# Kernel tuning notes

Hardware: AMD Instinct MI355X
Metric: run time of the kernel (lower is better)

Reference implementation:

```python
import jax, jax.numpy as jnp
import numpy as np

VAR0, VAR1 = 0.1, 0.2
THRESHOLD = 0.35
NEGPOS_RATIO = 7
LOW_GT_THRESH = 0.2  # match() filters GT whose best prior IoU < 0.2


def setup_inputs() -> dict:
    key = jax.random.key(0)
    ks = jax.random.split(key, 8)
    B, P, G = 16, 43008, 128
    loc_data = jax.random.normal(ks[0], (B, P, 4), jnp.float32)
    conf_data = jax.random.normal(ks[1], (B, P, 2), jnp.float32)
    landm_data = jax.random.normal(ks[2], (B, P, 10), jnp.float32)
    # priors in cxcywh form, positive sizes
    pc = jax.random.uniform(ks[3], (P, 2), jnp.float32)
    pwh = jax.random.uniform(ks[4], (P, 2), jnp.float32, minval=0.02, maxval=0.32)
    priors = jnp.concatenate([pc, pwh], axis=1)
    # targets: valid xyxy boxes + 10 landmark coords + label (face=1)
    ctr = jax.random.uniform(ks[5], (B, G, 2), jnp.float32, minval=0.2, maxval=0.8)
    wh = jax.random.uniform(ks[6], (B, G, 2), jnp.float32, minval=0.05, maxval=0.3)
    boxes = jnp.concatenate([ctr - wh / 2, ctr + wh / 2], axis=-1)
    landms = jax.random.uniform(ks[7], (B, G, 10), jnp.float32)
    labels = jnp.ones((B, G, 1), jnp.float32)
    targets = jnp.concatenate([boxes, landms, labels], axis=-1)
    return {"loc_data": loc_data, "conf_data": conf_data, "landm_data": landm_data,
            "priors": priors, "targets": targets}


def point_form(priors):
    return jnp.concatenate([priors[:, :2] - priors[:, 2:] / 2,
                            priors[:, :2] + priors[:, 2:] / 2], axis=1)


def jaccard(a, b):  # a: [G,4] xyxy, b: [P,4] xyxy -> [G,P]
    lt = jnp.maximum(a[:, None, :2], b[None, :, :2])
    rb = jnp.minimum(a[:, None, 2:], b[None, :, 2:])
    wh = jnp.clip(rb - lt, 0.0)
    inter = wh[..., 0] * wh[..., 1]
    area_a = (a[:, 2] - a[:, 0]) * (a[:, 3] - a[:, 1])
    area_b = (b[:, 2] - b[:, 0]) * (b[:, 3] - b[:, 1])
    return inter / (area_a[:, None] + area_b[None, :] - inter)


def encode(matched, priors):  # matched xyxy [P,4], priors cxcywh [P,4]
    g_cxcy = (matched[:, :2] + matched[:, 2:]) / 2 - priors[:, :2]
    g_cxcy = g_cxcy / (VAR0 * priors[:, 2:])
    g_wh = jnp.log((matched[:, 2:] - matched[:, :2]) / priors[:, 2:]) / VAR1
    return jnp.concatenate([g_cxcy, g_wh], axis=1)


def encode_landm(matched, priors):  # matched [P,10], priors [P,4]
    m = matched.reshape(-1, 5, 2)
    g = (m - priors[:, None, :2]) / (VAR0 * priors[:, None, 2:])
    return g.reshape(-1, 10)


def match_one(truths, labels, landms, priors):
    G = truths.shape[0]
    overlaps = jaccard(truths, point_form(priors))  # [G, P]
    best_prior_overlap = overlaps.max(axis=1)       # [G]
    best_prior_idx = overlaps.argmax(axis=1)        # [G]
    valid = best_prior_overlap >= LOW_GT_THRESH
    any_valid = jnp.any(valid)
    best_truth_overlap = overlaps.max(axis=0)       # [P]
    best_truth_idx = overlaps.argmax(axis=0)        # [P]
    # index_fill_(0, best_prior_idx_filter, 2): ensure each valid GT keeps its best prior
    fill_val = jnp.where(valid, 2.0, best_truth_overlap[best_prior_idx])
    best_truth_overlap = best_truth_overlap.at[best_prior_idx].set(fill_val)
    # best_truth_idx[best_prior_idx[j]] = j for all j
    best_truth_idx = best_truth_idx.at[best_prior_idx].set(jnp.arange(G))
    matches = truths[best_truth_idx]                       # [P,4]
    conf = labels[best_truth_idx].astype(jnp.int32)        # [P]
    conf = jnp.where(best_truth_overlap < THRESHOLD, 0, conf)
    conf = jnp.where(any_valid, conf, 0)  # no valid GT -> all background
    loc = encode(matches, priors)
    landm = encode_landm(landms[best_truth_idx], priors)
    return loc, conf, landm


def smooth_l1(x):
    ax = jnp.abs(x)
    return jnp.where(ax < 1.0, 0.5 * ax * ax, ax - 0.5)


def reference(loc_data, conf_data, landm_data, priors, targets):
    truths = targets[..., :4]
    landms = targets[..., 4:14]
    labels = targets[..., 14]
    loc_t, conf_t, landm_t = jax.vmap(
        lambda t, l, lm: match_one(t, l, lm, priors))(truths, labels, landms)

    # landmark loss over positives
    pos1 = conf_t > 0
    N1 = jnp.maximum(pos1.sum().astype(jnp.float32), 1.0)
    loss_landm = jnp.sum(smooth_l1(landm_data - landm_t) * pos1[..., None])

    # localization loss over positives
    pos = conf_t != 0
    num_pos = pos.sum(axis=1, keepdims=True)  # [B,1]
    loss_l = jnp.sum(smooth_l1(loc_data - loc_t) * pos[..., None])

    # hard negative mining on per-prior CE loss
    lse = jax.scipy.special.logsumexp(conf_data, axis=-1)  # [B,P]
    gathered = jnp.take_along_axis(conf_data, conf_t[..., None], axis=-1)[..., 0]
    ce_all = lse - gathered                                # [B,P] per-prior CE
    mine = jnp.where(pos, 0.0, ce_all)
    loss_idx = jnp.argsort(-mine, axis=1)
    idx_rank = jnp.argsort(loss_idx, axis=1)
    num_neg = jnp.clip(NEGPOS_RATIO * num_pos, None, pos.shape[1] - 1)
    neg = idx_rank < num_neg
    sel = pos | neg
    loss_c = jnp.sum(jnp.where(sel, ce_all, 0.0))

    N = jnp.maximum(num_pos.sum().astype(jnp.float32), 1.0)
    return loss_l / N, loss_c / N, loss_landm / N1
```

## Files before the change

kernel.cpp:

```cpp
#include <hip/hip_runtime.h>
#include <stdint.h>


#define GC 8
#define PPI 4

__device__ __forceinline__ float sl1(float x) {
  float a = fabsf(x);
  return a < 1.f ? 0.5f * a * a : a - 0.5f;
}

__device__ __forceinline__ double dwave(double v) {
#pragma unroll
  for (int o = 32; o; o >>= 1) v += __shfl_down(v, o);
  return v;
}

__global__ __launch_bounds__(256) void k_match(
    const float* __restrict__ priors, const float* __restrict__ targets,
    float* __restrict__ bto, int* __restrict__ bti,
    unsigned long long* __restrict__ bp, int P, int G, int NIOU, int PTI,
    int NGC, int PC) {
  int tid = threadIdx.x;
  __shared__ float4 sgt[128];
  __shared__ float sga[128];
  __shared__ unsigned long long sred[GC * 256];

  if ((int)blockIdx.x < NIOU) {
    int b = blockIdx.x / PTI, tile = blockIdx.x % PTI;
    int base = tile * (256 * PPI);
    for (int g = tid; g < G; g += 256) {
      const float* t = targets + ((size_t)b * G + g) * 15;
      float x1 = t[0], y1 = t[1], x2 = t[2], y2 = t[3];
      sgt[g] = make_float4(x1, y1, x2, y2);
      sga[g] = (x2 - x1) * (y2 - y1);
    }
    __syncthreads();

    float px1[PPI], py1[PPI], px2[PPI], py2[PPI], pa[PPI];
    float bi[PPI], sb[PPI];
    int bidx[PPI];
#pragma unroll
    for (int k = 0; k < PPI; ++k) {
      int p = base + tid + k * 256;
      int pl = p < P ? p : P - 1;
      float4 pr = ((const float4*)priors)[pl];
      px1[k] = pr.x - pr.z * 0.5f; py1[k] = pr.y - pr.w * 0.5f;
      px2[k] = pr.x + pr.z * 0.5f; py2[k] = pr.y + pr.w * 0.5f;
      pa[k] = pr.z * pr.w;
      bi[k] = 0.f; sb[k] = 1.f; bidx[k] = 0;
    }

#define IOU_BODY(T, A, GG)                                                 \
  {                                                                        \
    float iw = fminf(T.z, px2[k]) - fmaxf(T.x, px1[k]);                    \
    float ih = fminf(T.w, py2[k]) - fmaxf(T.y, py1[k]);                    \
    float inter = fmaxf(iw, 0.f) * ih;        \
    float S = A + pa[k];                                                   \
    if (inter * sb[k] > bi[k] * S) { bi[k] = inter; sb[k] = S; bidx[k] = GG; } \
  }

    for (int g = 0; g < G; g += 4) {
      float4 T0 = sgt[g], T1 = sgt[g + 1], T2 = sgt[g + 2], T3 = sgt[g + 3];
      float A0 = sga[g], A1 = sga[g + 1], A2 = sga[g + 2], A3 = sga[g + 3];
#pragma unroll
      for (int k = 0; k < PPI; ++k) {
        IOU_BODY(T0, A0, g)
        IOU_BODY(T1, A1, g + 1)
        IOU_BODY(T2, A2, g + 2)
        IOU_BODY(T3, A3, g + 3)
      }
    }
#undef IOU_BODY
#pragma unroll
    for (int k = 0; k < PPI; ++k) {
      int p = base + tid + k * 256;
      if (p < P) {
        bto[(size_t)b * P + p] = bi[k] / (sb[k] - bi[k]);
        bti[(size_t)b * P + p] = bidx[k];
      }
    }
  } else {
    int bc = blockIdx.x - NIOU;
    int pc = bc % PC;
    int gcb = (bc / PC) % NGC;
    int b = bc / (PC * NGC);
    int g0 = gcb * GC;

    if (tid < GC) {
      int g = g0 + tid;
      float4 v = make_float4(0.f, 0.f, 0.f, 0.f);
      if (g < G) {
        const float* t = targets + ((size_t)b * G + g) * 15;
        v = make_float4(t[0], t[1], t[2], t[3]);
      }
      sgt[tid] = v;
    }
    __syncthreads();

    float gx1[GC], gy1[GC], gx2[GC], gy2[GC], ga[GC];
#pragma unroll
    for (int j = 0; j < GC; ++j) {
      float4 T = sgt[j];
      gx1[j] = T.x; gy1[j] = T.y; gx2[j] = T.z; gy2[j] = T.w;
      ga[j] = (T.z - T.x) * (T.w - T.y);
    }

    int chunk = (P + PC - 1) / PC;
    int ps = pc * chunk;
    int pe = ps + chunk; if (pe > P) pe = P;
    int count = pe - ps;

    float bi[GC], sb[GC];
    unsigned bpp[GC];
#pragma unroll
    for (int j = 0; j < GC; ++j) { bi[j] = 0.f; sb[j] = 1.f; bpp[j] = (unsigned)(ps + tid); }

#define BP_BODY(X1, Y1, X2, Y2, AR, PP)                                     \
  {                                                                         \
    float iw = fminf(gx2[j], X2) - fmaxf(gx1[j], X1);                       \
    float ih = fminf(gy2[j], Y2) - fmaxf(gy1[j], Y1);                       \
    float inter = fmaxf(iw, 0.f) * ih;                                      \
    float S = ga[j] + AR;                                                   \
    if (inter * sb[j] > bi[j] * S) { bi[j] = inter; sb[j] = S; bpp[j] = (unsigned)PP; } \
  }

    for (int i = tid; i < count; i += 1024) {
      int p0 = ps + i;
      int i1 = i + 256, i2 = i + 512, i3 = i + 768;
      int p1 = (i1 < count) ? ps + i1 : p0;
      int p2 = (i2 < count) ? ps + i2 : p0;
      int p3 = (i3 < count) ? ps + i3 : p0;
      float4 q0 = ((const float4*)priors)[p0];
      float4 q1 = ((const float4*)priors)[p1];
      float4 q2 = ((const float4*)priors)[p2];
      float4 q3 = ((const float4*)priors)[p3];
      float ax1 = q0.x - q0.z * 0.5f, ay1 = q0.y - q0.w * 0.5f;
      float ax2 = q0.x + q0.z * 0.5f, ay2 = q0.y + q0.w * 0.5f;
      float aa = q0.z * q0.w;
      float bx1 = q1.x - q1.z * 0.5f, by1 = q1.y - q1.w * 0.5f;
      float bx2 = q1.x + q1.z * 0.5f, by2 = q1.y + q1.w * 0.5f;
      float ba = q1.z * q1.w;
      float cx1 = q2.x - q2.z * 0.5f, cy1 = q2.y - q2.w * 0.5f;
      float cx2 = q2.x + q2.z * 0.5f, cy2 = q2.y + q2.w * 0.5f;
      float ca = q2.z * q2.w;
      float dx1 = q3.x - q3.z * 0.5f, dy1 = q3.y - q3.w * 0.5f;
      float dx2 = q3.x + q3.z * 0.5f, dy2 = q3.y + q3.w * 0.5f;
      float da = q3.z * q3.w;
#pragma unroll
      for (int j = 0; j < GC; ++j) {
        BP_BODY(ax1, ay1, ax2, ay2, aa, p0)
        BP_BODY(bx1, by1, bx2, by2, ba, p1)
        BP_BODY(cx1, cy1, cx2, cy2, ca, p2)
        BP_BODY(dx1, dy1, dx2, dy2, da, p3)
      }
    }
#undef BP_BODY

#pragma unroll
    for (int j = 0; j < GC; ++j) {
      float iou = bi[j] / (sb[j] - bi[j]);
      unsigned long long pk =
          ((unsigned long long)__float_as_uint(iou) << 32) | (unsigned)(~bpp[j]);
      sred[j * 256 + tid] = pk;
    }
    __syncthreads();
    {
      int j = tid >> 5, s = tid & 31;
      unsigned long long m = sred[j * 256 + s];
#pragma unroll
      for (int t = 1; t < 8; ++t) {
        unsigned long long v = sred[j * 256 + s + t * 32];
        if (v > m) m = v;
      }
      __syncthreads();
      sred[j * 256 + s] = m;
    }
    __syncthreads();
    if (tid < GC) {
      unsigned long long m = sred[tid * 256];
      for (int s = 1; s < 32; ++s) {
        unsigned long long v = sred[tid * 256 + s];
        if (v > m) m = v;
      }
      int g = g0 + tid;
      if (g < G) atomicMax(&bp[(size_t)b * G + g], m);
    }
  }
}

__global__ void k_scatter(const unsigned long long* __restrict__ bp,
                          float* __restrict__ bto, int* __restrict__ bti,
                          int* __restrict__ anyv, int P, int G) {
  int b = blockIdx.x, g = threadIdx.x;
  __shared__ unsigned spp[128];
  __shared__ int s_any;
  if (g == 0) s_any = 0;
  __syncthreads();
  unsigned long long m = bp[(size_t)b * G + g];
  unsigned pp = ~(unsigned)m;
  float val = __uint_as_float((unsigned)(m >> 32));
  bool ok = (m != 0ULL);
  float oldv = 0.f;
  if (ok) oldv = bto[(size_t)b * P + pp];
  spp[g] = ok ? pp : 0xFFFFFFFFu;
  if (ok && val >= 0.2f) s_any = 1;
  __syncthreads();
  bool win = ok;
  for (int g2 = g + 1; g2 < G; ++g2)
    if (spp[g2] == pp) win = false;
  if (win) {
    bto[(size_t)b * P + pp] = (val >= 0.2f) ? 2.0f : oldv;
    bti[(size_t)b * P + pp] = g;
  }
  __syncthreads();
  if (g == 0) anyv[b] = s_any;
}

__global__ __launch_bounds__(256) void k_main(
    const float* __restrict__ loc, const float* __restrict__ conf,
    const float* __restrict__ lm, const float* __restrict__ priors,
    const float* __restrict__ targets, const float* __restrict__ bto,
    const int* __restrict__ bti, const int* __restrict__ anyv,
    float* __restrict__ mine, unsigned* __restrict__ h1,
    double* __restrict__ pll, double* __restrict__ pllm,
    double* __restrict__ plc, double* __restrict__ msum,
    int* __restrict__ pnp, int P, int G, int PT) {
  int b = blockIdx.x / PT, tile = blockIdx.x % PT;
  int tid = threadIdx.x;
  int p = tile * 256 + tid;

  __shared__ float st[128 * 15];
  __shared__ unsigned hist[1024];
  __shared__ double rs[16];
  __shared__ int ri[4];

  for (int i = tid; i < G * 15; i += 256) st[i] = targets[(size_t)b * G * 15 + i];
  for (int i = tid; i < 1024; i += 256) hist[i] = 0;
  __syncthreads();

  double ll = 0, llm = 0, lc = 0, ms = 0;
  int np = 0;
  if (p < P) {
    size_t idx = (size_t)b * P + p;
    int av = anyv[b];
    float ov = bto[idx];
    int ti = bti[idx];
    bool pos = av && (ov >= 0.35f);

    float2 c = ((const float2*)conf)[idx];
    float mx = fmaxf(c.x, c.y);
    float lse = mx + logf(expf(c.x - mx) + expf(c.y - mx));
    float ce = lse - (pos ? c.y : c.x);
    float mv = pos ? 0.f : ce;
    mine[idx] = mv;
    ms = (double)mv;
    atomicAdd(&hist[__float_as_uint(mv) >> 21], 1u);

    if (pos) {
      np = 1;
      lc = (double)ce;
      float4 pr = ((const float4*)priors)[p];
      const float* t = st + ti * 15;
      float dx = 0.1f * pr.z, dy = 0.1f * pr.w;
      float gx = ((t[0] + t[2]) * 0.5f - pr.x) / dx;
      float gy = ((t[1] + t[3]) * 0.5f - pr.y) / dy;
      float gw = logf((t[2] - t[0]) / pr.z) * 5.0f;
      float gh = logf((t[3] - t[1]) / pr.w) * 5.0f;
      float4 ld = ((const float4*)loc)[idx];
      ll = (double)(sl1(ld.x - gx) + sl1(ld.y - gy) + sl1(ld.z - gw) +
                    sl1(ld.w - gh));
      const float2* lmd = (const float2*)lm + idx * 5;
      float s = 0.f;
#pragma unroll
      for (int j = 0; j < 5; ++j) {
        float2 lv = lmd[j];
        float ex = (t[4 + 2 * j] - pr.x) / dx;
        float ey = (t[5 + 2 * j] - pr.y) / dy;
        s += sl1(lv.x - ex) + sl1(lv.y - ey);
      }
      llm = (double)s;
    }
  }

  ll = dwave(ll);
  llm = dwave(llm);
  lc = dwave(lc);
  ms = dwave(ms);
#pragma unroll
  for (int o = 32; o; o >>= 1) np += __shfl_down(np, o);
  int lane = tid & 63, wid = tid >> 6;
  if (lane == 0) {
    rs[wid] = ll; rs[4 + wid] = llm; rs[8 + wid] = lc; rs[12 + wid] = ms;
    ri[wid] = np;
  }
  __syncthreads();
  if (tid == 0) {
    pll[blockIdx.x] = rs[0] + rs[1] + rs[2] + rs[3];
    pllm[blockIdx.x] = rs[4] + rs[5] + rs[6] + rs[7];
    plc[blockIdx.x] = rs[8] + rs[9] + rs[10] + rs[11];
    msum[blockIdx.x] = rs[12] + rs[13] + rs[14] + rs[15];
    pnp[blockIdx.x] = ri[0] + ri[1] + ri[2] + ri[3];
  }
  for (int i = tid; i < 1024; i += 256)
    if (hist[i]) atomicAdd(&h1[(size_t)b * 1024 + i], hist[i]);
}

__global__ __launch_bounds__(1024) void k_tail(
    const unsigned* __restrict__ h1, const int* __restrict__ pnp,
    const double* __restrict__ msum, const float* __restrict__ mine,
    int* __restrict__ num_pos, double* __restrict__ pfs_b, int P, int PT) {
  int b = blockIdx.x, tid = threadIdx.x;
  __shared__ double sm[1024];
  __shared__ int sn[1024];
  __shared__ unsigned S[1024];
  __shared__ unsigned hs[2048];
  __shared__ int spf1, sk1, spf21, sk2;
  __shared__ unsigned stb;
  __shared__ double stie;
  __shared__ double rs[16];

  int n = 0;
  double m = 0;
  for (int i = tid; i < PT; i += 1024) { n += pnp[b * PT + i]; m += msum[b * PT + i]; }
  sn[tid] = n; sm[tid] = m;
  __syncthreads();
  for (int off = 512; off; off >>= 1) {
    if (tid < off) { sn[tid] += sn[tid + off]; sm[tid] += sm[tid + off]; }
    __syncthreads();
  }
  int npos = sn[0];
  if (tid == 0) num_pos[b] = npos;

  long long k = 7LL * (long long)npos;
  long long cap = P - 1;
  if (k <= 0) return;
  if (k >= cap) {
    if (tid == 0) pfs_b[b] = sm[0];
    return;
  }

  const float* mrow = mine + (size_t)b * P;

  {
    unsigned own = h1[(size_t)b * 1024 + tid];
    S[tid] = own;
    __syncthreads();
    for (int off = 1; off < 1024; off <<= 1) {
      unsigned add = (tid + off < 1024) ? S[tid + off] : 0;
      __syncthreads();
      S[tid] += add;
      __syncthreads();
    }
    int cnt = __syncthreads_count((long long)S[tid] >= k);
    int seg = cnt - 1;
    if (tid == seg) {
      long long cum = (seg + 1 < 1024) ? (long long)S[seg + 1] : 0;
      spf1 = seg;
      sk1 = (int)(k - cum);
    }
  }
  __syncthreads();
  int pf = spf1;

  hs[tid] = 0; hs[tid + 1024] = 0;
  __syncthreads();
  for (int base = 0; base < P; base += 4096) {
    int i0 = base + tid;
    int i1 = i0 + 1024, i2 = i0 + 2048, i3 = i0 + 3072;
    unsigned b0 = (i0 < P) ? __float_as_uint(mrow[i0]) : 0u;
    unsigned b1 = (i1 < P) ? __float_as_uint(mrow[i1]) : 0u;
    unsigned b2 = (i2 < P) ? __float_as_uint(mrow[i2]) : 0u;
    unsigned b3 = (i3 < P) ? __float_as_uint(mrow[i3]) : 0u;
    if (i0 < P && (int)(b0 >> 21) == pf) atomicAdd(&hs[(b0 >> 10) & 2047], 1u);
    if (i1 < P && (int)(b1 >> 21) == pf) atomicAdd(&hs[(b1 >> 10) & 2047], 1u);
    if (i2 < P && (int)(b2 >> 21) == pf) atomicAdd(&hs[(b2 >> 10) & 2047], 1u);
    if (i3 < P && (int)(b3 >> 21) == pf) atomicAdd(&hs[(b3 >> 10) & 2047], 1u);
  }
  __syncthreads();
  {
    unsigned h0 = hs[tid * 2], h1v = hs[tid * 2 + 1];
    S[tid] = h0 + h1v;
    __syncthreads();
    for (int off = 1; off < 1024; off <<= 1) {
      unsigned add = (tid + off < 1024) ? S[tid + off] : 0;
      __syncthreads();
      S[tid] += add;
      __syncthreads();
    }
    long long kk = (long long)sk1;
    int cnt = __syncthreads_count((long long)S[tid] >= kk);
    int seg = cnt - 1;
    if (tid == seg) {
      long long cum = (seg + 1 < 1024) ? (long long)S[seg + 1] : 0;
      int bin = seg * 2;
      if (cum + h1v >= kk) bin = seg * 2 + 1;
      else cum += h1v;
      spf21 = (pf << 11) | bin;
      sk2 = (int)(kk - cum);
    }
  }
  __syncthreads();
  int pf21 = spf21;

  hs[tid] = 0;
  __syncthreads();
  for (int base = 0; base < P; base += 4096) {
    int i0 = base + tid;
    int i1 = i0 + 1024, i2 = i0 + 2048, i3 = i0 + 3072;
    unsigned b0 = (i0 < P) ? __float_as_uint(mrow[i0]) : 0u;
    unsigned b1 = (i1 < P) ? __float_as_uint(mrow[i1]) : 0u;
    unsigned b2 = (i2 < P) ? __float_as_uint(mrow[i2]) : 0u;
    unsigned b3 = (i3 < P) ? __float_as_uint(mrow[i3]) : 0u;
    if (i0 < P && (int)(b0 >> 10) == pf21) atomicAdd(&hs[b0 & 1023], 1u);
    if (i1 < P && (int)(b1 >> 10) == pf21) atomicAdd(&hs[b1 & 1023], 1u);
    if (i2 < P && (int)(b2 >> 10) == pf21) atomicAdd(&hs[b2 & 1023], 1u);
    if (i3 < P && (int)(b3 >> 10) == pf21) atomicAdd(&hs[b3 & 1023], 1u);
  }
  __syncthreads();
  {
    unsigned own = hs[tid];
    S[tid] = own;
    __syncthreads();
    for (int off = 1; off < 1024; off <<= 1) {
      unsigned add = (tid + off < 1024) ? S[tid + off] : 0;
      __syncthreads();
      S[tid] += add;
      __syncthreads();
    }
    long long kk = (long long)sk2;
    int cnt = __syncthreads_count((long long)S[tid] >= kk);
    int seg = cnt - 1;
    if (tid == seg) {
      long long cum = (seg + 1 < 1024) ? (long long)S[seg + 1] : 0;
      unsigned tb = ((unsigned)pf21 << 10) | (unsigned)seg;
      stb = tb;
      stie = (double)(kk - cum) * (double)__uint_as_float(tb);
    }
  }
  __syncthreads();

  unsigned tb = stb;
  double v = 0.0;
  for (int base = 0; base < P; base += 4096) {
    int i0 = base + tid;
    int i1 = i0 + 1024, i2 = i0 + 2048, i3 = i0 + 3072;
    unsigned b0 = (i0 < P) ? __float_as_uint(mrow[i0]) : 0u;
    unsigned b1 = (i1 < P) ? __float_as_uint(mrow[i1]) : 0u;
    unsigned b2 = (i2 < P) ? __float_as_uint(mrow[i2]) : 0u;
    unsigned b3 = (i3 < P) ? __float_as_uint(mrow[i3]) : 0u;
    if (b0 > tb) v += (double)__uint_as_float(b0);
    if (b1 > tb) v += (double)__uint_as_float(b1);
    if (b2 > tb) v += (double)__uint_as_float(b2);
    if (b3 > tb) v += (double)__uint_as_float(b3);
  }
  v = dwave(v);
  int lane = tid & 63, wid = tid >> 6;
  if (lane == 0) rs[wid] = v;
  __syncthreads();
  if (tid == 0) {
    double t = 0;
    for (int i = 0; i < 16; ++i) t += rs[i];
    pfs_b[b] = t + stie;
  }
}

__global__ __launch_bounds__(256) void k_fin(
    const double* __restrict__ pll, const double* __restrict__ pllm,
    const double* __restrict__ plc, const double* __restrict__ pfs_b,
    const int* __restrict__ num_pos, float* __restrict__ out, int NBm, int B) {
  int tid = threadIdx.x;
  double a = 0, c = 0, d = 0, f = 0, n = 0;
  for (int i = tid; i < NBm; i += 256) { a += pll[i]; c += pllm[i]; d += plc[i]; }
  for (int i = tid; i < B; i += 256) { f += pfs_b[i]; n += (double)num_pos[i]; }
  a = dwave(a); c = dwave(c); d = dwave(d); f = dwave(f); n = dwave(n);
  __shared__ double rs[5 * 4];
  int lane = tid & 63, wid = tid >> 6;
  if (lane == 0) {
    rs[wid] = a; rs[4 + wid] = c; rs[8 + wid] = d;
    rs[12 + wid] = f; rs[16 + wid] = n;
  }
  __syncthreads();
  if (tid == 0) {
    double A = rs[0] + rs[1] + rs[2] + rs[3];
    double C = rs[4] + rs[5] + rs[6] + rs[7];
    double D = rs[8] + rs[9] + rs[10] + rs[11];
    double F = rs[12] + rs[13] + rs[14] + rs[15];
    double N = rs[16] + rs[17] + rs[18] + rs[19];
    if (N < 1.0) N = 1.0;
    out[0] = (float)(A / N);
    out[1] = (float)((D + F) / N);
    out[2] = (float)(C / N);
  }
}

extern "C" void kernel_launch(void* const* d_in, const int* in_sizes, int n_in,
                              void* d_out, int out_size, void* d_ws,
                              size_t ws_size, hipStream_t stream) {
  const float* loc = (const float*)d_in[0];
  const float* conf = (const float*)d_in[1];
  const float* lm = (const float*)d_in[2];
  const float* priors = (const float*)d_in[3];
  const float* targets = (const float*)d_in[4];

  int P = in_sizes[3] / 4;
  int B = in_sizes[0] / (4 * P);
  int G = in_sizes[4] / (15 * B);
  int PT = (P + 255) / 256;
  int PTI = (P + 256 * PPI - 1) / (256 * PPI);
  int NBm = B * PT;
  int NGC = (G + GC - 1) / GC;
  int PC = 8;
  int NIOU = B * PTI;
  int NBP = B * NGC * PC;

  char* w = (char*)d_ws;
  size_t off = 0;
  unsigned long long* bp = (unsigned long long*)(w + off);
  off += (size_t)B * G * 8;
  double* pfs_b = (double*)(w + off);
  off += (size_t)B * 8;
  int* ctrl = (int*)(w + off);
  off += (size_t)(2 * B) * 4;
  int* anyv = ctrl;
  int* num_pos = ctrl + B;
  unsigned* h1 = (unsigned*)(w + off);
  off += (size_t)B * 1024 * 4;
  size_t clear_bytes = off;
  off = (off + 255) & ~(size_t)255;
  float* bto = (float*)(w + off);
  off += (size_t)B * P * 4;
  int* bti = (int*)(w + off);
  off += (size_t)B * P * 4;
  float* mine = (float*)(w + off);
  off += (size_t)B * P * 4;
  double* pll = (double*)(w + off);
  off += (size_t)NBm * 8;
  double* pllm = (double*)(w + off);
  off += (size_t)NBm * 8;
  double* plc = (double*)(w + off);
  off += (size_t)NBm * 8;
  double* msum = (double*)(w + off);
  off += (size_t)NBm * 8;
  int* pnp = (int*)(w + off);
  off += (size_t)NBm * 4;

  hipMemsetAsync(d_ws, 0, clear_bytes, stream);

  k_match<<<NIOU + NBP, 256, 0, stream>>>(priors, targets, bto, bti, bp, P, G,
                                          NIOU, PTI, NGC, PC);
  k_scatter<<<B, G, 0, stream>>>(bp, bto, bti, anyv, P, G);
  k_main<<<B * PT, 256, 0, stream>>>(loc, conf, lm, priors, targets, bto, bti,
                                     anyv, mine, h1, pll, pllm, plc, msum, pnp,
                                     P, G, PT);
  k_tail<<<B, 1024, 0, stream>>>(h1, pnp, msum, mine, num_pos, pfs_b, P, PT);
  k_fin<<<1, 256, 0, stream>>>(pll, pllm, plc, pfs_b, num_pos, (float*)d_out,
                               NBm, B);
}
```

Measured before the change: 178.8 us.

## Fuse per-prior loss computation into IoU match kernel with delta correction pass

The per-prior loss work (CE, mining value, loc and landmark smooth-L1) now runs in the IoU matching blocks right after best-GT selection, which removes the separate k_main pass that re-read bto/bti. A new k_fix kernel applies the forced best-prior matches afterwards by computing per-batch deltas (old versus new assignment) to the partial sums and patching the mining array. The mining histogram moves into k_tail, which rescans the mine row itself, and final reduction work shifts into k_tail, leaving k_fin with only per-batch values. This trades one full launch and memory pass for a histogram rescan and delta bookkeeping, and the fused IoU blocks now run more memory work alongside the compute-bound matching.

Result: no change. 177.9 us (-0.5%).

```diff
diff --git a/kernel.cpp b/kernel.cpp
--- a/kernel.cpp
+++ b/kernel.cpp
@@ -16,19 +16,28 @@
   return v;
 }
 
-__global__ __launch_bounds__(256) void k_match(
+__global__ __launch_bounds__(256) void k_mm(
     const float* __restrict__ priors, const float* __restrict__ targets,
-    float* __restrict__ bto, int* __restrict__ bti,
-    unsigned long long* __restrict__ bp, int P, int G, int NIOU, int PTI,
-    int NGC, int PC) {
+    const float* __restrict__ loc, const float* __restrict__ conf,
+    const float* __restrict__ lm, float* __restrict__ bto,
+    int* __restrict__ bti, unsigned long long* __restrict__ bp,
+    float* __restrict__ mine, double* __restrict__ pll,
+    double* __restrict__ pllm, double* __restrict__ plc,
+    double* __restrict__ msum, int* __restrict__ pnp, int P, int G, int NIOU,
+    int PTI, int NGC, int PC) {
   int tid = threadIdx.x;
+  __shared__ char smem[16384];
   __shared__ float4 sgt[128];
   __shared__ float sga[128];
-  __shared__ unsigned long long sred[GC * 256];
 
   if ((int)blockIdx.x < NIOU) {
+    float* st = (float*)smem;
+    double* rs = (double*)(smem + 7680);
+    int* ri = (int*)(smem + 7808);
     int b = blockIdx.x / PTI, tile = blockIdx.x % PTI;
     int base = tile * (256 * PPI);
+    for (int i = tid; i < G * 15; i += 256)
+      st[i] = targets[(size_t)b * G * 15 + i];
     for (int g = tid; g < G; g += 256) {
       const float* t = targets + ((size_t)b * G + g) * 15;
       float x1 = t[0], y1 = t[1], x2 = t[2], y2 = t[3];
@@ -55,11 +64,10 @@
   {                                                                        \
     float iw = fminf(T.z, px2[k]) - fmaxf(T.x, px1[k]);                    \
     float ih = fminf(T.w, py2[k]) - fmaxf(T.y, py1[k]);                    \
-    float inter = fmaxf(iw, 0.f) * ih;        \
+    float inter = fmaxf(iw, 0.f) * ih;                                     \
     float S = A + pa[k];                                                   \
     if (inter * sb[k] > bi[k] * S) { bi[k] = inter; sb[k] = S; bidx[k] = GG; } \
   }
-
     for (int g = 0; g < G; g += 4) {
       float4 T0 = sgt[g], T1 = sgt[g + 1], T2 = sgt[g + 2], T3 = sgt[g + 3];
       float A0 = sga[g], A1 = sga[g + 1], A2 = sga[g + 2], A3 = sga[g + 3];
@@ -72,15 +80,73 @@
       }
     }
 #undef IOU_BODY
+
+    double ll = 0, llm = 0, lc = 0, ms = 0;
+    int np = 0;
 #pragma unroll
     for (int k = 0; k < PPI; ++k) {
       int p = base + tid + k * 256;
       if (p < P) {
-        bto[(size_t)b * P + p] = bi[k] / (sb[k] - bi[k]);
-        bti[(size_t)b * P + p] = bidx[k];
+        size_t idx = (size_t)b * P + p;
+        float ov = bi[k] / (sb[k] - bi[k]);
+        int ti = bidx[k];
+        bto[idx] = ov;
+        bti[idx] = ti;
+        bool pos = ov >= 0.35f;
+        float2 c = ((const float2*)conf)[idx];
+        float mx = fmaxf(c.x, c.y);
+        float dd = fabsf(c.x - c.y);
+        float lse = mx + logf(1.f + expf(-dd));
+        float ce = lse - (pos ? c.y : c.x);
+        float mv = pos ? 0.f : ce;
+        mine[idx] = mv;
+        ms += (double)mv;
+        if (pos) {
+          np++;
+          lc += (double)ce;
+          float4 pr = ((const float4*)priors)[p];
+          const float* t = st + ti * 15;
+          float rz = 1.f / pr.z, rw = 1.f / pr.w;
+          float rdx = 10.f * rz, rdy = 10.f * rw;
+          float gx = ((t[0] + t[2]) * 0.5f - pr.x) * rdx;
+          float gy = ((t[1] + t[3]) * 0.5f - pr.y) * rdy;
+          float gw = logf((t[2] - t[0]) * rz) * 5.0f;
+          float gh = logf((t[3] - t[1]) * rw) * 5.0f;
+          float4 ld = ((const float4*)loc)[idx];
+          ll += (double)(sl1(ld.x - gx) + sl1(ld.y - gy) + sl1(ld.z - gw) +
+                         sl1(ld.w - gh));
+          const float2* lmd = (const float2*)lm + idx * 5;
+          float s = 0.f;
+#pragma unroll
+          for (int j = 0; j < 5; ++j) {
+            float2 lv = lmd[j];
+            float ex = (t[4 + 2 * j] - pr.x) * rdx;
+            float ey = (t[5 + 2 * j] - pr.y) * rdy;
+            s += sl1(lv.x - ex) + sl1(lv.y - ey);
+          }
+          llm += (double)s;
+        }
       }
     }
+
+    ll = dwave(ll); llm = dwave(llm); lc = dwave(lc); ms = dwave(ms);
+#pragma unroll
+    for (int o = 32; o; o >>= 1) np += __shfl_down(np, o);
+    int lane = tid & 63, wid = tid >> 6;
+    if (lane == 0) {
+      rs[wid] = ll; rs[4 + wid] = llm; rs[8 + wid] = lc; rs[12 + wid] = ms;
+      ri[wid] = np;
+    }
+    __syncthreads();
+    if (tid == 0) {
+      pll[blockIdx.x] = rs[0] + rs[1] + rs[2] + rs[3];
+      pllm[blockIdx.x] = rs[4] + rs[5] + rs[6] + rs[7];
+      plc[blockIdx.x] = rs[8] + rs[9] + rs[10] + rs[11];
+      msum[blockIdx.x] = rs[12] + rs[13] + rs[14] + rs[15];
+      pnp[blockIdx.x] = ri[0] + ri[1] + ri[2] + ri[3];
+    }
   } else {
+    unsigned long long* sred = (unsigned long long*)smem;
     int bc = blockIdx.x - NIOU;
     int pc = bc % PC;
     int gcb = (bc / PC) % NGC;
@@ -124,7 +190,6 @@
     float S = ga[j] + AR;                                                   \
     if (inter * sb[j] > bi[j] * S) { bi[j] = inter; sb[j] = S; bpp[j] = (unsigned)PP; } \
   }
-
     for (int i = tid; i < count; i += 1024) {
       int p0 = ps + i;
       int i1 = i + 256, i2 = i + 512, i3 = i + 768;
@@ -189,162 +254,184 @@
   }
 }
 
-__global__ void k_scatter(const unsigned long long* __restrict__ bp,
-                          float* __restrict__ bto, int* __restrict__ bti,
-                          int* __restrict__ anyv, int P, int G) {
+__global__ void k_fix(const unsigned long long* __restrict__ bp,
+                      const float* __restrict__ bto, const int* __restrict__ bti,
+                      const float* __restrict__ conf, const float* __restrict__ loc,
+                      const float* __restrict__ lm, const float* __restrict__ priors,
+                      const float* __restrict__ targets, float* __restrict__ mine,
+                      int* __restrict__ anyv, double* __restrict__ dacc,
+                      int* __restrict__ dnpb, int P, int G) {
   int b = blockIdx.x, g = threadIdx.x;
   __shared__ unsigned spp[128];
-  __shared__ int s_any;
-  if (g == 0) s_any = 0;
-  __syncthreads();
+  __shared__ double sd[128 * 4];
+  __shared__ int si[128];
+
   unsigned long long m = bp[(size_t)b * G + g];
   unsigned pp = ~(unsigned)m;
   float val = __uint_as_float((unsigned)(m >> 32));
-  bool ok = (m != 0ULL);
-  float oldv = 0.f;
-  if (ok) oldv = bto[(size_t)b * P + pp];
-  spp[g] = ok ? pp : 0xFFFFFFFFu;
-  if (ok && val >= 0.2f) s_any = 1;
-  __syncthreads();
-  bool win = ok;
+  spp[g] = pp;
+  bool valid = val >= 0.2f;
+  int av = __syncthreads_or(valid ? 1 : 0);
+  if (g == 0) anyv[b] = av;
+
+  bool win = true;
   for (int g2 = g + 1; g2 < G; ++g2)
-    if (spp[g2] == pp) win = false;
+    if (spp[g2] == pp) { win = false; break; }
+
+  double dll = 0, dllm = 0, dlc = 0, dms = 0;
+  int dnp = 0;
   if (win) {
-    bto[(size_t)b * P + pp] = (val >= 0.2f) ? 2.0f : oldv;
-    bti[(size_t)b * P + pp] = g;
-  }
-  __syncthreads();
-  if (g == 0) anyv[b] = s_any;
-}
-
-__global__ __launch_bounds__(256) void k_main(
-    const float* __restrict__ loc, const float* __restrict__ conf,
-    const float* __restrict__ lm, const float* __restrict__ priors,
-    const float* __restrict__ targets, const float* __restrict__ bto,
-    const int* __restrict__ bti, const int* __restrict__ anyv,
-    float* __restrict__ mine, unsigned* __restrict__ h1,
-    double* __restrict__ pll, double* __restrict__ pllm,
-    double* __restrict__ plc, double* __restrict__ msum,
-    int* __restrict__ pnp, int P, int G, int PT) {
-  int b = blockIdx.x / PT, tile = blockIdx.x % PT;
-  int tid = threadIdx.x;
-  int p = tile * 256 + tid;
-
-  __shared__ float st[128 * 15];
-  __shared__ unsigned hist[1024];
-  __shared__ double rs[16];
-  __shared__ int ri[4];
-
-  for (int i = tid; i < G * 15; i += 256) st[i] = targets[(size_t)b * G * 15 + i];
-  for (int i = tid; i < 1024; i += 256) hist[i] = 0;
-  __syncthreads();
-
-  double ll = 0, llm = 0, lc = 0, ms = 0;
-  int np = 0;
-  if (p < P) {
-    size_t idx = (size_t)b * P + p;
-    int av = anyv[b];
-    float ov = bto[idx];
-    int ti = bti[idx];
-    bool pos = av && (ov >= 0.35f);
+    size_t idx = (size_t)b * P + pp;
+    float ov_o = bto[idx];
+    int ti_o = bti[idx];
+    float ov_n = valid ? 2.0f : ov_o;
+    int ti_n = g;
+    bool pos_o = ov_o >= 0.35f, pos_n = ov_n >= 0.35f;
 
     float2 c = ((const float2*)conf)[idx];
     float mx = fmaxf(c.x, c.y);
-    float lse = mx + logf(expf(c.x - mx) + expf(c.y - mx));
-    float ce = lse - (pos ? c.y : c.x);
-    float mv = pos ? 0.f : ce;
-    mine[idx] = mv;
-    ms = (double)mv;
-    atomicAdd(&hist[__float_as_uint(mv) >> 21], 1u);
-
-    if (pos) {
-      np = 1;
-      lc = (double)ce;
-      float4 pr = ((const float4*)priors)[p];
-      const float* t = st + ti * 15;
-      float dx = 0.1f * pr.z, dy = 0.1f * pr.w;
-      float gx = ((t[0] + t[2]) * 0.5f - pr.x) / dx;
-      float gy = ((t[1] + t[3]) * 0.5f - pr.y) / dy;
-      float gw = logf((t[2] - t[0]) / pr.z) * 5.0f;
-      float gh = logf((t[3] - t[1]) / pr.w) * 5.0f;
+    float dd = fabsf(c.x - c.y);
+    float lse = mx + logf(1.f + expf(-dd));
+    float ce_o = lse - (pos_o ? c.y : c.x);
+    float ce_n = lse - (pos_n ? c.y : c.x);
+    float mv_o = mine[idx];
+    float mv_n = pos_n ? 0.f : ce_n;
+    if (mv_n != mv_o) mine[idx] = mv_n;
+    dms = (double)mv_n - (double)mv_o;
+    dnp = (pos_n ? 1 : 0) - (pos_o ? 1 : 0);
+    dlc = (pos_n ? (double)ce_n : 0.0) - (pos_o ? (double)ce_o : 0.0);
+
+    if (pos_o || pos_n) {
+      float4 pr = ((const float4*)priors)[pp];
+      float rz = 1.f / pr.z, rw = 1.f / pr.w;
+      float rdx = 10.f * rz, rdy = 10.f * rw;
       float4 ld = ((const float4*)loc)[idx];
-      ll = (double)(sl1(ld.x - gx) + sl1(ld.y - gy) + sl1(ld.z - gw) +
-                    sl1(ld.w - gh));
       const float2* lmd = (const float2*)lm + idx * 5;
-      float s = 0.f;
-#pragma unroll
-      for (int j = 0; j < 5; ++j) {
-        float2 lv = lmd[j];
-        float ex = (t[4 + 2 * j] - pr.x) / dx;
-        float ey = (t[5 + 2 * j] - pr.y) / dy;
-        s += sl1(lv.x - ex) + sl1(lv.y - ey);
+      float2 lv[5];
+#pragma unroll
+      for (int j = 0; j < 5; ++j) lv[j] = lmd[j];
+      for (int pass = 0; pass < 2; ++pass) {
+        bool act = pass ? pos_n : pos_o;
+        int ti = pass ? ti_n : ti_o;
+        if (!act) continue;
+        const float* t = targets + ((size_t)b * G + ti) * 15;
+        float gx = ((t[0] + t[2]) * 0.5f - pr.x) * rdx;
+        float gy = ((t[1] + t[3]) * 0.5f - pr.y) * rdy;
+        float gw = logf((t[2] - t[0]) * rz) * 5.0f;
+        float gh = logf((t[3] - t[1]) * rw) * 5.0f;
+        double l = (double)(sl1(ld.x - gx) + sl1(ld.y - gy) +
+                            sl1(ld.z - gw) + sl1(ld.w - gh));
+        float s = 0.f;
+#pragma unroll
+        for (int j = 0; j < 5; ++j) {
+          float ex = (t[4 + 2 * j] - pr.x) * rdx;
+          float ey = (t[5 + 2 * j] - pr.y) * rdy;
+          s += sl1(lv[j].x - ex) + sl1(lv[j].y - ey);
+        }
+        if (pass) { dll += l; dllm += (double)s; }
+        else { dll -= l; dllm -= (double)s; }
       }
-      llm = (double)s;
-    }
-  }
-
-  ll = dwave(ll);
-  llm = dwave(llm);
-  lc = dwave(lc);
-  ms = dwave(ms);
-#pragma unroll
-  for (int o = 32; o; o >>= 1) np += __shfl_down(np, o);
-  int lane = tid & 63, wid = tid >> 6;
-  if (lane == 0) {
-    rs[wid] = ll; rs[4 + wid] = llm; rs[8 + wid] = lc; rs[12 + wid] = ms;
-    ri[wid] = np;
-  }
-  __syncthreads();
-  if (tid == 0) {
-    pll[blockIdx.x] = rs[0] + rs[1] + rs[2] + rs[3];
-    pllm[blockIdx.x] = rs[4] + rs[5] + rs[6] + rs[7];
-    plc[blockIdx.x] = rs[8] + rs[9] + rs[10] + rs[11];
-    msum[blockIdx.x] = rs[12] + rs[13] + rs[14] + rs[15];
-    pnp[blockIdx.x] = ri[0] + ri[1] + ri[2] + ri[3];
-  }
-  for (int i = tid; i < 1024; i += 256)
-    if (hist[i]) atomicAdd(&h1[(size_t)b * 1024 + i], hist[i]);
+    }
+  }
+  sd[g] = dll; sd[128 + g] = dllm; sd[256 + g] = dlc; sd[384 + g] = dms;
+  si[g] = dnp;
+  __syncthreads();
+  for (int off = 64; off; off >>= 1) {
+    if (g < off) {
+      sd[g] += sd[g + off]; sd[128 + g] += sd[128 + g + off];
+      sd[256 + g] += sd[256 + g + off]; sd[384 + g] += sd[384 + g + off];
+      si[g] += si[g + off];
+    }
+    __syncthreads();
+  }
+  if (g == 0) {
+    dacc[b * 4 + 0] = sd[0]; dacc[b * 4 + 1] = sd[128];
+    dacc[b * 4 + 2] = sd[256]; dacc[b * 4 + 3] = sd[384];
+    dnpb[b] = si[0];
+  }
 }
 
 __global__ __launch_bounds__(1024) void k_tail(
-    const unsigned* __restrict__ h1, const int* __restrict__ pnp,
-    const double* __restrict__ msum, const float* __restrict__ mine,
-    int* __restrict__ num_pos, double* __restrict__ pfs_b, int P, int PT) {
+    const int* __restrict__ pnp, const double* __restrict__ msum,
+    const double* __restrict__ pll, const double* __restrict__ pllm,
+    const double* __restrict__ plc, const double* __restrict__ dacc,
+    const int* __restrict__ dnpb, const int* __restrict__ anyv,
+    const float* __restrict__ mine, int* __restrict__ num_pos,
+    double* __restrict__ pllb, double* __restrict__ pllmb,
+    double* __restrict__ plcb, double* __restrict__ pfs_b, int P, int PTI) {
   int b = blockIdx.x, tid = threadIdx.x;
-  __shared__ double sm[1024];
-  __shared__ int sn[1024];
+  __shared__ double rs[16 * 5];
+  __shared__ int ris[16];
   __shared__ unsigned S[1024];
   __shared__ unsigned hs[2048];
   __shared__ int spf1, sk1, spf21, sk2;
   __shared__ unsigned stb;
   __shared__ double stie;
-  __shared__ double rs[16];
-
+
+  double a = 0, cc = 0, d = 0, ms = 0;
   int n = 0;
-  double m = 0;
-  for (int i = tid; i < PT; i += 1024) { n += pnp[b * PT + i]; m += msum[b * PT + i]; }
-  sn[tid] = n; sm[tid] = m;
-  __syncthreads();
-  for (int off = 512; off; off >>= 1) {
-    if (tid < off) { sn[tid] += sn[tid + off]; sm[tid] += sm[tid + off]; }
-    __syncthreads();
-  }
-  int npos = sn[0];
-  if (tid == 0) num_pos[b] = npos;
+  for (int i = tid; i < PTI; i += 1024) {
+    int ix = b * PTI + i;
+    a += pll[ix]; cc += pllm[ix]; d += plc[ix]; ms += msum[ix]; n += pnp[ix];
+  }
+  a = dwave(a); cc = dwave(cc); d = dwave(d); ms = dwave(ms);
+#pragma unroll
+  for (int o = 32; o; o >>= 1) n += __shfl_down(n, o);
+  int lane = tid & 63, wid = tid >> 6;
+  if (lane == 0) {
+    rs[wid] = a; rs[16 + wid] = cc; rs[32 + wid] = d; rs[48 + wid] = ms;
+    ris[wid] = n;
+  }
+  __syncthreads();
+  int npos = 0;
+  double A = 0, C = 0, D = 0, MS = 0;
+  if (tid == 0) {
+    for (int i = 0; i < 16; ++i) {
+      A += rs[i]; C += rs[16 + i]; D += rs[32 + i]; MS += rs[48 + i];
+      npos += ris[i];
+    }
+    A += dacc[b * 4 + 0]; C += dacc[b * 4 + 1]; D += dacc[b * 4 + 2];
+    MS += dacc[b * 4 + 3];
+    npos += dnpb[b];
+    if (!anyv[b]) { A = 0; C = 0; D = 0; npos = 0; }
+    num_pos[b] = npos;
+    pllb[b] = A; pllmb[b] = C; plcb[b] = D;
+    ris[0] = npos;
+    rs[48] = MS;
+  }
+  __syncthreads();
+  npos = ris[0];
+  MS = rs[48];
 
   long long k = 7LL * (long long)npos;
   long long cap = P - 1;
-  if (k <= 0) return;
+  if (k <= 0) {
+    if (tid == 0) pfs_b[b] = 0.0;
+    return;
+  }
   if (k >= cap) {
-    if (tid == 0) pfs_b[b] = sm[0];
+    if (tid == 0) pfs_b[b] = MS;
     return;
   }
 
   const float* mrow = mine + (size_t)b * P;
-
+  hs[tid] = 0;
+  __syncthreads();
+  for (int base = 0; base < P; base += 4096) {
+    int i0 = base + tid;
+    int i1 = i0 + 1024, i2 = i0 + 2048, i3 = i0 + 3072;
+    unsigned b0 = (i0 < P) ? __float_as_uint(mrow[i0]) : 0xFFFFFFFFu;
+    unsigned b1 = (i1 < P) ? __float_as_uint(mrow[i1]) : 0xFFFFFFFFu;
+    unsigned b2 = (i2 < P) ? __float_as_uint(mrow[i2]) : 0xFFFFFFFFu;
+    unsigned b3 = (i3 < P) ? __float_as_uint(mrow[i3]) : 0xFFFFFFFFu;
+    if (b0 != 0xFFFFFFFFu) atomicAdd(&hs[b0 >> 21], 1u);
+    if (b1 != 0xFFFFFFFFu) atomicAdd(&hs[b1 >> 21], 1u);
+    if (b2 != 0xFFFFFFFFu) atomicAdd(&hs[b2 >> 21], 1u);
+    if (b3 != 0xFFFFFFFFu) atomicAdd(&hs[b3 >> 21], 1u);
+  }
+  __syncthreads();
   {
-    unsigned own = h1[(size_t)b * 1024 + tid];
-    S[tid] = own;
+    S[tid] = hs[tid];
     __syncthreads();
     for (int off = 1; off < 1024; off <<= 1) {
       unsigned add = (tid + off < 1024) ? S[tid + off] : 0;
@@ -419,8 +506,7 @@
   }
   __syncthreads();
   {
-    unsigned own = hs[tid];
-    S[tid] = own;
+    S[tid] = hs[tid];
     __syncthreads();
     for (int off = 1; off < 1024; off <<= 1) {
       unsigned add = (tid + off < 1024) ? S[tid + off] : 0;
@@ -455,7 +541,6 @@
     if (b3 > tb) v += (double)__uint_as_float(b3);
   }
   v = dwave(v);
-  int lane = tid & 63, wid = tid >> 6;
   if (lane == 0) rs[wid] = v;
   __syncthreads();
   if (tid == 0) {
@@ -465,28 +550,18 @@
   }
 }
 
-__global__ __launch_bounds__(256) void k_fin(
-    const double* __restrict__ pll, const double* __restrict__ pllm,
-    const double* __restrict__ plc, const double* __restrict__ pfs_b,
-    const int* __restrict__ num_pos, float* __restrict__ out, int NBm, int B) {
-  int tid = threadIdx.x;
-  double a = 0, c = 0, d = 0, f = 0, n = 0;
-  for (int i = tid; i < NBm; i += 256) { a += pll[i]; c += pllm[i]; d += plc[i]; }
-  for (int i = tid; i < B; i += 256) { f += pfs_b[i]; n += (double)num_pos[i]; }
-  a = dwave(a); c = dwave(c); d = dwave(d); f = dwave(f); n = dwave(n);
-  __shared__ double rs[5 * 4];
-  int lane = tid & 63, wid = tid >> 6;
-  if (lane == 0) {
-    rs[wid] = a; rs[4 + wid] = c; rs[8 + wid] = d;
-    rs[12 + wid] = f; rs[16 + wid] = n;
-  }
-  __syncthreads();
-  if (tid == 0) {
-    double A = rs[0] + rs[1] + rs[2] + rs[3];
-    double C = rs[4] + rs[5] + rs[6] + rs[7];
-    double D = rs[8] + rs[9] + rs[10] + rs[11];
-    double F = rs[12] + rs[13] + rs[14] + rs[15];
-    double N = rs[16] + rs[17] + rs[18] + rs[19];
+__global__ void k_fin(const double* __restrict__ pllb,
+                      const double* __restrict__ pllmb,
+                      const double* __restrict__ plcb,
+                      const double* __restrict__ pfs_b,
+                      const int* __restrict__ num_pos, float* __restrict__ out,
+                      int B) {
+  if (threadIdx.x == 0) {
+    double A = 0, C = 0, D = 0, F = 0, N = 0;
+    for (int i = 0; i < B; ++i) {
+      A += pllb[i]; C += pllmb[i]; D += plcb[i]; F += pfs_b[i];
+      N += (double)num_pos[i];
+    }
     if (N < 1.0) N = 1.0;
     out[0] = (float)(A / N);
     out[1] = (float)((D + F) / N);
@@ -506,26 +581,16 @@
   int P = in_sizes[3] / 4;
   int B = in_sizes[0] / (4 * P);
   int G = in_sizes[4] / (15 * B);
-  int PT = (P + 255) / 256;
   int PTI = (P + 256 * PPI - 1) / (256 * PPI);
-  int NBm = B * PT;
+  int NIOU = B * PTI;
   int NGC = (G + GC - 1) / GC;
   int PC = 8;
-  int NIOU = B * PTI;
   int NBP = B * NGC * PC;
 
   char* w = (char*)d_ws;
   size_t off = 0;
   unsigned long long* bp = (unsigned long long*)(w + off);
   off += (size_t)B * G * 8;
-  double* pfs_b = (double*)(w + off);
-  off += (size_t)B * 8;
-  int* ctrl = (int*)(w + off);
-  off += (size_t)(2 * B) * 4;
-  int* anyv = ctrl;
-  int* num_pos = ctrl + B;
-  unsigned* h1 = (unsigned*)(w + off);
-  off += (size_t)B * 1024 * 4;
   size_t clear_bytes = off;
   off = (off + 255) & ~(size_t)255;
   float* bto = (float*)(w + off);
@@ -535,25 +600,43 @@
   float* mine = (float*)(w + off);
   off += (size_t)B * P * 4;
   double* pll = (double*)(w + off);
-  off += (size_t)NBm * 8;
+  off += (size_t)NIOU * 8;
   double* pllm = (double*)(w + off);
-  off += (size_t)NBm * 8;
+  off += (size_t)NIOU * 8;
   double* plc = (double*)(w + off);
-  off += (size_t)NBm * 8;
+  off += (size_t)NIOU * 8;
   double* msum = (double*)(w + off);
-  off += (size_t)NBm * 8;
+  off += (size_t)NIOU * 8;
   int* pnp = (int*)(w + off);
-  off += (size_t)NBm * 4;
+  off += (size_t)NIOU * 4;
+  off = (off + 7) & ~(size_t)7;
+  double* dacc = (double*)(w + off);
+  off += (size_t)B * 4 * 8;
+  double* pllb = (double*)(w + off);
+  off += (size_t)B * 8;
+  double* pllmb = (double*)(w + off);
+  off += (size_t)B * 8;
+  double* plcb = (double*)(w + off);
+  off += (size_t)B * 8;
+  double* pfs_b = (double*)(w + off);
+  off += (size_t)B * 8;
+  int* dnpb = (int*)(w + off);
+  off += (size_t)B * 4;
+  int* anyv = (int*)(w + off);
+  off += (size_t)B * 4;
+  int* num_pos = (int*)(w + off);
+  off += (size_t)B * 4;
 
   hipMemsetAsync(d_ws, 0, clear_bytes, stream);
 
-  k_match<<<NIOU + NBP, 256, 0, stream>>>(priors, targets, bto, bti, bp, P, G,
-                                          NIOU, PTI, NGC, PC);
-  k_scatter<<<B, G, 0, stream>>>(bp, bto, bti, anyv, P, G);
-  k_main<<<B * PT, 256, 0, stream>>>(loc, conf, lm, priors, targets, bto, bti,
-                                     anyv, mine, h1, pll, pllm, plc, msum, pnp,
-                                     P, G, PT);
-  k_tail<<<B, 1024, 0, stream>>>(h1, pnp, msum, mine, num_pos, pfs_b, P, PT);
-  k_fin<<<1, 256, 0, stream>>>(pll, pllm, plc, pfs_b, num_pos, (float*)d_out,
-                               NBm, B);
+  k_mm<<<NIOU + NBP, 256, 0, stream>>>(priors, targets, loc, conf, lm, bto,
+                                       bti, bp, mine, pll, pllm, plc, msum,
+                                       pnp, P, G, NIOU, PTI, NGC, PC);
+  k_fix<<<B, G, 0, stream>>>(bp, bto, bti, conf, loc, lm, priors, targets,
+                             mine, anyv, dacc, dnpb, P, G);
+  k_tail<<<B, 1024, 0, stream>>>(pnp, msum, pll, pllm, plc, dacc, dnpb, anyv,
+                                 mine, num_pos, pllb, pllmb, plcb, pfs_b, P,
+                                 PTI);
+  k_fin<<<1, 64, 0, stream>>>(pllb, pllmb, plcb, pfs_b, num_pos,
+                              (float*)d_out, B);
 }
```
